# Optimization experiments

Measured on AMD Instinct MI355X. Metric: run time of the kernel, lower is better.

The kernel has to match this reference:

```python
import jax, jax.numpy as jnp
import numpy as np

N = 20000          # nodes (== virtual nodes, forced by scatter dim_size + residuals)
E = 240000         # edges
H = 256            # hidden_dim
SD = 128           # scalar_dim (mult of 0e in "128x0e+64x1o+32x2e")
FEAT = 128 + 64 * 3 + 32 * 5   # 480 = target_irreps dim
C = 4              # vn_channel


def _lin(key, din, dout):
    k1, k2 = jax.random.split(key)
    s = 1.0 / np.sqrt(din)
    w = jax.random.uniform(k1, (din, dout), jnp.float32, -s, s)
    b = jax.random.uniform(k2, (dout,), jnp.float32, -s, s)
    return w, b


def _mlp(x, w1, b1, w2, b2):
    # BaseMLP: Linear -> SiLU -> Linear (no norm, no residual, no last act)
    return jax.nn.silu(x @ w1 + b1) @ w2 + b2


def setup_inputs() -> dict:
    key = jax.random.key(0)
    ks = jax.random.split(key, 12)
    inp = {
        "node_feat": jax.random.normal(ks[0], (N, FEAT), jnp.float32),
        "node_pos": jax.random.normal(ks[1], (N, 3), jnp.float32),
        "vn_feat": jax.random.normal(ks[2], (N, H), jnp.float32),
        "vn_pos": jax.random.normal(ks[3], (N, 3 * C), jnp.float32),
        "edge_index": jax.random.randint(ks[4], (2, E), 0, N),
        "w_scalar": jax.random.normal(ks[5], (SD, SD), jnp.float32),  # e3nn o3.Linear 0e->0e path
    }
    mlps = {"cm": (SD + H + C * C, H), "vr": (H, C), "rv": (H, C * C),
            "ft": (H, H), "f2t": (H, SD), "vf": (H, H)}
    i = 6
    for name, (din, dout) in mlps.items():
        k1, k2 = jax.random.split(ks[i]); i += 1
        inp[name + "_w1"], inp[name + "_b1"] = _lin(k1, din, H)
        inp[name + "_w2"], inp[name + "_b2"] = _lin(k2, H, dout)
    return inp


def reference(node_feat, node_pos, vn_feat, vn_pos, edge_index, w_scalar,
              cm_w1, cm_b1, cm_w2, cm_b2, vr_w1, vr_b1, vr_w2, vr_b2,
              rv_w1, rv_b1, rv_w2, rv_b2, ft_w1, ft_b1, ft_w2, ft_b2,
              f2t_w1, f2t_b1, f2t_w2, f2t_b2, vf_w1, vf_b1, vf_w2, vf_b2):
    n = node_feat.shape[0]
    row, col = edge_index[0], edge_index[1]

    # e3nn o3.Linear(target_irreps -> SDx0e): single 0e->0e path, 1/sqrt(fan_in)
    nfs = (node_feat[:, :SD] @ w_scalar) * (1.0 / np.sqrt(SD))

    # per-edge relative positions between node pos (tiled to C channels) and vn pos
    d = (jnp.tile(node_pos[row], (1, C)) - vn_pos[col]).reshape(-1, C, 3)  # [E,C,3]

    # normalized gram matrix of the C difference vectors
    ip = jnp.einsum('ecj,ekj->eck', d, d).reshape(-1, C * C)
    ip = ip / jnp.maximum(jnp.linalg.norm(ip, axis=-1, keepdims=True), 1e-8)

    dn = d / jnp.maximum(jnp.linalg.norm(d, axis=-1, keepdims=True), 1e-8)  # [E,C,3]

    msg = _mlp(jnp.concatenate([nfs[row], vn_feat[col], ip], axis=1),
               cm_w1, cm_b1, cm_w2, cm_b2)                                   # [E,H]

    w_vr = _mlp(msg, vr_w1, vr_b1, vr_w2, vr_b2)                 # [E,C]
    w_rv = _mlp(msg, rv_w1, rv_b1, rv_w2, rv_b2).reshape(-1, C, C)

    inv = 1.0 / np.sqrt(C)
    # FCTP Cx1o (x) 1x0e -> 1x1o  (x2 == 1): weighted sum of the C vectors
    vr_upd = inv * jnp.einsum('ec,ecj->ej', w_vr, dn)            # [E,3]
    # FCTP Cx1o (x) 1x0e -> Cx1o on -dn
    rv_upd = inv * jnp.einsum('ecu,ecj->euj', w_rv, -dn).reshape(-1, 3 * C)  # [E,3C]

    cnt = jnp.maximum(jax.ops.segment_sum(jnp.ones((row.shape[0],), msg.dtype), row, n), 1.0)[:, None]
    agg_feat = jax.ops.segment_sum(msg, row, n) / cnt            # scatter_mean by row
    agg_vr = jax.ops.segment_sum(vr_upd, row, n) / cnt
    agg_rv = jax.ops.segment_sum(rv_upd, row, n) / cnt

    ds = _mlp(_mlp(agg_feat, ft_w1, ft_b1, ft_w2, ft_b2), f2t_w1, f2t_b1, f2t_w2, f2t_b2)
    node_feat_out = node_feat.at[:, :SD].add(ds)  # delta only hits the scalar (0e) block
    node_pos_out = node_pos + agg_vr
    vn_feat_out = vn_feat + _mlp(agg_feat, vf_w1, vf_b1, vf_w2, vf_b2)
    vn_pos_out = vn_pos + agg_rv
    return node_feat_out, node_pos_out, vn_feat_out, vn_pos_out
```

## Files before the change

kernel.cpp:

```cpp
#include <hip/hip_runtime.h>
#include <hip/hip_bf16.h>
#include <math.h>


#define FEAT 480
#define HDIM 256
#define SDIM 128
#define MSTR 264

#define OW1   0
#define OW2   106496
#define OVR1  172032
#define ORV1  237568
#define OVR2  303104
#define ORV2  307200
#define OFT1  311296
#define OFT2  376832
#define OF2T1 442368
#define OF2T2 507904
#define OVF1  540672
#define OVF2  606208
#define OWTOT 671744

#define NB_WPREP 2624
#define NB_VNB   5000
#define NB_NFS   625

typedef __attribute__((ext_vector_type(8))) short bf16x8;
typedef __attribute__((ext_vector_type(4))) float f32x4;

__device__ __forceinline__ float rcp_f(float x) {
    return __builtin_amdgcn_rcpf(x);
}
__device__ __forceinline__ float silu_f(float x) {
    return x * rcp_f(1.0f + __expf(-x));
}
__device__ __forceinline__ ushort f2b(float v) {
    __hip_bfloat16 h = __float2bfloat16(v);
    return *(ushort*)&h;
}
__device__ __forceinline__ float b2f(ushort u) {
    union { unsigned int i; float f; } c;
    c.i = ((unsigned int)u) << 16;
    return c.f;
}

#define KLOOP2(SRC, WP)                                                        \
    {                                                                          \
        _Pragma("unroll")                                                      \
        for (int mt = 0; mt < 4; ++mt)                                         \
            _Pragma("unroll")                                                  \
            for (int nt = 0; nt < 2; ++nt) acc[mt][nt] = (f32x4)0.f;           \
        __builtin_amdgcn_s_setprio(1);                                         \
        _Pragma("unroll")                                                      \
        for (int ks = 0; ks < 8; ++ks) {                                       \
            bf16x8 a_[4];                                                      \
            _Pragma("unroll")                                                  \
            for (int mt = 0; mt < 4; ++mt)                                     \
                a_[mt] = *(const bf16x8*)&(SRC)[(mt * 16 + lr) * MSTR + ks * 32 + lk * 8]; \
            _Pragma("unroll")                                                  \
            for (int nt = 0; nt < 2; ++nt) {                                   \
                const bf16x8 b = *(const bf16x8*)&(WP)[(size_t)(((wv * 2 + nt) * 8 + ks) * 512) + lane * 8]; \
                _Pragma("unroll")                                              \
                for (int mt = 0; mt < 4; ++mt)                                 \
                    acc[mt][nt] = __builtin_amdgcn_mfma_f32_16x16x32_bf16(a_[mt], b, acc[mt][nt], 0, 0, 0); \
            }                                                                  \
        }                                                                      \
        __builtin_amdgcn_s_setprio(0);                                         \
    }

#define EPI_SILU2(DST, BIAS)                                                   \
    _Pragma("unroll")                                                          \
    for (int nt = 0; nt < 2; ++nt) {                                           \
        const int col = colBase + nt * 16 + lr;                                \
        const float bb = (BIAS)[col];                                          \
        _Pragma("unroll")                                                      \
        for (int mt = 0; mt < 4; ++mt)                                         \
            _Pragma("unroll")                                                  \
            for (int r = 0; r < 4; ++r) {                                      \
                const int row = mt * 16 + lk * 4 + r;                          \
                (DST)[row * MSTR + col] = f2b(silu_f(acc[mt][nt][r] + bb));    \
            }                                                                  \
    }

#define KLOOP_FR(SRC, WP)                                                      \
    {                                                                          \
        _Pragma("unroll")                                                      \
        for (int mt = 0; mt < 2; ++mt)                                         \
            _Pragma("unroll")                                                  \
            for (int nt = 0; nt < 4; ++nt) accn[mt][nt] = (f32x4)0.f;          \
        _Pragma("unroll")                                                      \
        for (int ks = 0; ks < 8; ++ks) {                                       \
            const bf16x8 a0 = *(const bf16x8*)&(SRC)[lr * MSTR + ks * 32 + lk * 8];        \
            const bf16x8 a1 = *(const bf16x8*)&(SRC)[(lr + 16) * MSTR + ks * 32 + lk * 8]; \
            _Pragma("unroll")                                                  \
            for (int nt = 0; nt < 4; ++nt) {                                   \
                const bf16x8 b = *(const bf16x8*)&(WP)[(size_t)(((wv * 4 + nt) * 8 + ks) * 512) + lane * 8]; \
                accn[0][nt] = __builtin_amdgcn_mfma_f32_16x16x32_bf16(a0, b, accn[0][nt], 0, 0, 0); \
                accn[1][nt] = __builtin_amdgcn_mfma_f32_16x16x32_bf16(a1, b, accn[1][nt], 0, 0, 0); \
            }                                                                  \
        }                                                                      \
    }

#define EPI_SILUN(DST, BIAS)                                                   \
    _Pragma("unroll")                                                          \
    for (int nt = 0; nt < 4; ++nt) {                                           \
        const int col = colBase + nt * 16 + lr;                                \
        const float bb = (BIAS)[col];                                          \
        _Pragma("unroll")                                                      \
        for (int mt = 0; mt < 2; ++mt)                                         \
            _Pragma("unroll")                                                  \
            for (int r = 0; r < 4; ++r) {                                      \
                const int row = mt * 16 + lk * 4 + r;                          \
                (DST)[row * MSTR + col] = f2b(silu_f(accn[mt][nt][r] + bb));   \
            }                                                                  \
    }

__global__ __launch_bounds__(256) void k_prep(
    const float* __restrict__ w1, const float* __restrict__ w2,
    const float* __restrict__ vrw1, const float* __restrict__ rvw1,
    const float* __restrict__ vrw2, const float* __restrict__ rvw2,
    const float* __restrict__ ftw1, const float* __restrict__ ftw2,
    const float* __restrict__ f2tw1, const float* __restrict__ f2tw2,
    const float* __restrict__ vfw1, const float* __restrict__ vfw2,
    ushort* __restrict__ wb,
    const float* __restrict__ vn_feat, ushort* __restrict__ vnb,
    const float* __restrict__ node_feat, const float* __restrict__ w_scalar,
    ushort* __restrict__ nfsb,
    const int* __restrict__ eidx, int* __restrict__ cnt_i, int E)
{
    __shared__ float At[32][20];
    __shared__ float Wt[16][128];
    const int bid = blockIdx.x;
    const int t = threadIdx.x;

    if (bid < NB_WPREP) {
        const int idx = bid * 256 + t;
        ushort v;
        if (idx < OW2) {
            const int o = idx, f = o >> 9, l = (o >> 3) & 63, e = o & 7;
            const int nt = f / 13, ks = f % 13;
            const int col = nt * 16 + (l & 15);
            const int k = ks * 32 + ((l >> 4) << 3) + e;
            v = (k < 400) ? f2b(w1[(size_t)k * 256 + col]) : (ushort)0;
        } else if (idx < OVR1) {
            const int o = idx - OW2, f = o >> 9, l = (o >> 3) & 63, e = o & 7;
            const int col = (f >> 3) * 16 + (l & 15);
            const int k = (f & 7) * 32 + ((l >> 4) << 3) + e;
            v = f2b(w2[(size_t)k * 256 + col]);
        } else if (idx < ORV1) {
            const int o = idx - OVR1, f = o >> 9, l = (o >> 3) & 63, e = o & 7;
            const int col = (f >> 3) * 16 + (l & 15);
            const int k = (f & 7) * 32 + ((l >> 4) << 3) + e;
            v = f2b(vrw1[(size_t)k * 256 + col]);
        } else if (idx < OVR2) {
            const int o = idx - ORV1, f = o >> 9, l = (o >> 3) & 63, e = o & 7;
            const int col = (f >> 3) * 16 + (l & 15);
            const int k = (f & 7) * 32 + ((l >> 4) << 3) + e;
            v = f2b(rvw1[(size_t)k * 256 + col]);
        } else if (idx < ORV2) {
            const int o = idx - OVR2, f = o >> 9, l = (o >> 3) & 63, e = o & 7;
            const int col = l & 15;
            const int k = f * 32 + ((l >> 4) << 3) + e;
            v = (col < 4) ? f2b(vrw2[(size_t)k * 4 + col]) : (ushort)0;
        } else if (idx < OFT1) {
            const int o = idx - ORV2, f = o >> 9, l = (o >> 3) & 63, e = o & 7;
            const int col = l & 15;
            const int k = f * 32 + ((l >> 4) << 3) + e;
            v = f2b(rvw2[(size_t)k * 16 + col]);
        } else if (idx < OFT2) {
            const int o = idx - OFT1, f = o >> 9, l = (o >> 3) & 63, e = o & 7;
            const int col = (f >> 3) * 16 + (l & 15);
            const int k = (f & 7) * 32 + ((l >> 4) << 3) + e;
            v = f2b(ftw1[(size_t)k * 256 + col]);
        } else if (idx < OF2T1) {
            const int o = idx - OFT2, f = o >> 9, l = (o >> 3) & 63, e = o & 7;
            const int col = (f >> 3) * 16 + (l & 15);
            const int k = (f & 7) * 32 + ((l >> 4) << 3) + e;
            v = f2b(ftw2[(size_t)k * 256 + col]);
        } else if (idx < OF2T2) {
            const int o = idx - OF2T1, f = o >> 9, l = (o >> 3) & 63, e = o & 7;
            const int col = (f >> 3) * 16 + (l & 15);
            const int k = (f & 7) * 32 + ((l >> 4) << 3) + e;
            v = f2b(f2tw1[(size_t)k * 256 + col]);
        } else if (idx < OVF1) {
            const int o = idx - OF2T2, f = o >> 9, l = (o >> 3) & 63, e = o & 7;
            const int col = (f >> 3) * 16 + (l & 15);
            const int k = (f & 7) * 32 + ((l >> 4) << 3) + e;
            v = f2b(f2tw2[(size_t)k * 128 + col]);
        } else if (idx < OVF2) {
            const int o = idx - OVF1, f = o >> 9, l = (o >> 3) & 63, e = o & 7;
            const int col = (f >> 3) * 16 + (l & 15);
            const int k = (f & 7) * 32 + ((l >> 4) << 3) + e;
            v = f2b(vfw1[(size_t)k * 256 + col]);
        } else {
            const int o = idx - OVF2, f = o >> 9, l = (o >> 3) & 63, e = o & 7;
            const int col = (f >> 3) * 16 + (l & 15);
            const int k = (f & 7) * 32 + ((l >> 4) << 3) + e;
            v = f2b(vfw2[(size_t)k * 256 + col]);
        }
        wb[idx] = v;
    } else if (bid < NB_WPREP + NB_VNB) {
        const int i = (bid - NB_WPREP) * 256 + t;
        const float4 v = *(const float4*)&vn_feat[(size_t)i * 4];
        ushort4 o;
        o.x = f2b(v.x); o.y = f2b(v.y); o.z = f2b(v.z); o.w = f2b(v.w);
        *(ushort4*)&vnb[(size_t)i * 4] = o;
    } else if (bid < NB_WPREP + NB_VNB + NB_NFS) {
        const int m0 = (bid - NB_WPREP - NB_VNB) * 32;
        const int c4 = (t & 31) * 4;
        const int rg = t >> 5;
        float acc[4][4] = {};
        for (int k0 = 0; k0 < 128; k0 += 16) {
            if (t < 128) {
                const int r = t >> 2, kk = (t & 3) * 4;
                *(float4*)&At[r][kk] =
                    *(const float4*)&node_feat[(size_t)(m0 + r) * FEAT + k0 + kk];
            }
            #pragma unroll
            for (int i = 0; i < 2; ++i) {
                const int p  = t + i * 256;
                const int wr = p >> 5, wc = (p & 31) * 4;
                *(float4*)&Wt[wr][wc] =
                    *(const float4*)&w_scalar[(size_t)(k0 + wr) * SDIM + wc];
            }
            __syncthreads();
            #pragma unroll
            for (int kk = 0; kk < 16; ++kk) {
                const float4 w = *(const float4*)&Wt[kk][c4];
                #pragma unroll
                for (int j = 0; j < 4; ++j) {
                    const float a = At[rg * 4 + j][kk];
                    acc[j][0] = fmaf(a, w.x, acc[j][0]);
                    acc[j][1] = fmaf(a, w.y, acc[j][1]);
                    acc[j][2] = fmaf(a, w.z, acc[j][2]);
                    acc[j][3] = fmaf(a, w.w, acc[j][3]);
                }
            }
            __syncthreads();
        }
        const float s = 0.08838834764831845f;
        #pragma unroll
        for (int j = 0; j < 4; ++j) {
            ushort4 o;
            o.x = f2b(acc[j][0] * s); o.y = f2b(acc[j][1] * s);
            o.z = f2b(acc[j][2] * s); o.w = f2b(acc[j][3] * s);
            *(ushort4*)&nfsb[(size_t)(m0 + rg * 4 + j) * SDIM + c4] = o;
        }
    } else {
        const int e = (bid - NB_WPREP - NB_VNB - NB_NFS) * 256 + t;
        if (e < E) atomicAdd(&cnt_i[eidx[e]], 1);
    }
}

__global__ __launch_bounds__(1024) void k_scanA(
    const int* __restrict__ cnt_i, int* __restrict__ rowstart,
    float* __restrict__ cntf, int* __restrict__ bsum, int Nn)
{
    __shared__ int sh[1024];
    const int t = threadIdx.x;
    const int i = blockIdx.x * 1024 + t;
    const int v = (i < Nn) ? cnt_i[i] : 0;
    sh[t] = v;
    __syncthreads();
    for (int off = 1; off < 1024; off <<= 1) {
        const int add = (t >= off) ? sh[t - off] : 0;
        __syncthreads();
        sh[t] += add;
        __syncthreads();
    }
    if (i < Nn) {
        rowstart[i + 1] = sh[t];
        cntf[i] = fmaxf((float)v, 1.0f);
    }
    if (t == 1023) bsum[blockIdx.x] = sh[t];
}

__global__ __launch_bounds__(1024) void k_scanC(
    int* __restrict__ rowstart, const int* __restrict__ bsum, int Nn)
{
    __shared__ int carry_s;
    const int t = threadIdx.x;
    if (t == 0) {
        int s = 0;
        for (int b = 0; b < (int)blockIdx.x; ++b) s += bsum[b];
        carry_s = s;
    }
    __syncthreads();
    const int i = blockIdx.x * 1024 + t;
    if (i < Nn) rowstart[i + 1] += carry_s;
    if (i == 0) rowstart[0] = 0;
}

__global__ __launch_bounds__(256) void k_place(
    const int* __restrict__ eidx, const int* __restrict__ rowstart,
    int* __restrict__ cursor, int* __restrict__ elist, int E)
{
    const int e = blockIdx.x * 256 + threadIdx.x;
    if (e < E) {
        const int r = eidx[e];
        const int p = atomicAdd(&cursor[r], 1);
        elist[rowstart[r] + p] = e;
    }
}

__global__ __launch_bounds__(512, 4) void k_edge(
    const ushort* __restrict__ nfsb, const ushort* __restrict__ vnb,
    const float* __restrict__ node_pos, const float* __restrict__ vn_pos,
    const int* __restrict__ eidx, const int* __restrict__ elist,
    const ushort* __restrict__ wb,
    const float* __restrict__ b1, const float* __restrict__ b2,
    const float* __restrict__ vrb1, const float* __restrict__ vrb2,
    const float* __restrict__ rvb1, const float* __restrict__ rvb2,
    float* __restrict__ agg_feat, float* __restrict__ agg_vr,
    float* __restrict__ agg_rv, int E)
{
    __shared__ ushort Mg[64 * MSTR];
    __shared__ ushort Hd[64 * MSTR];
    __shared__ ushort ipB[64 * 16];
    __shared__ float dnS[64][12];
    __shared__ float wvrS[64][4];
    __shared__ float wrvS[64][16];
    __shared__ int rowi[64], coli[64];

    const int t  = threadIdx.x;
    const int nwg = E / 64;
    const int q = nwg >> 3, rr8 = nwg & 7;
    const int xcd = blockIdx.x & 7, pos = blockIdx.x >> 3;
    const int bswz = (xcd < rr8 ? xcd * (q + 1) : rr8 * (q + 1) + (xcd - rr8) * q) + pos;
    const int e0 = bswz * 64;
    const int wv = t >> 6;
    const int lane = t & 63;
    const int lr = lane & 15;
    const int lk = lane >> 4;
    const int colBase = wv * 32;

    if (t < 64) {
        const int e = elist[e0 + t];
        const int r = eidx[e];
        const int c = eidx[E + e];
        rowi[t] = r; coli[t] = c;
        const float px = node_pos[r * 3 + 0];
        const float py = node_pos[r * 3 + 1];
        const float pz = node_pos[r * 3 + 2];
        float d[4][3];
        #pragma unroll
        for (int ch = 0; ch < 4; ++ch) {
            d[ch][0] = px - vn_pos[(size_t)c * 12 + ch * 3 + 0];
            d[ch][1] = py - vn_pos[(size_t)c * 12 + ch * 3 + 1];
            d[ch][2] = pz - vn_pos[(size_t)c * 12 + ch * 3 + 2];
        }
        float ss = 0.f, ipv[16];
        #pragma unroll
        for (int ci = 0; ci < 4; ++ci)
            #pragma unroll
            for (int ck = 0; ck < 4; ++ck) {
                const float v = d[ci][0]*d[ck][0] + d[ci][1]*d[ck][1] + d[ci][2]*d[ck][2];
                ipv[ci * 4 + ck] = v; ss += v * v;
            }
        const float inrm = rcp_f(fmaxf(sqrtf(ss), 1e-8f));
        #pragma unroll
        for (int i = 0; i < 16; ++i) ipB[t * 16 + i] = f2b(ipv[i] * inrm);
        #pragma unroll
        for (int ch = 0; ch < 4; ++ch) {
            const float nn = sqrtf(d[ch][0]*d[ch][0] + d[ch][1]*d[ch][1] + d[ch][2]*d[ch][2]);
            const float s = rcp_f(fmaxf(nn, 1e-8f));
            dnS[t][ch * 3 + 0] = d[ch][0] * s;
            dnS[t][ch * 3 + 1] = d[ch][1] * s;
            dnS[t][ch * 3 + 2] = d[ch][2] * s;
        }
    }
    __syncthreads();

    const ushort* nA[4]; const ushort* vA[4];
    #pragma unroll
    for (int mt = 0; mt < 4; ++mt) {
        nA[mt] = nfsb + (size_t)rowi[mt * 16 + lr] * SDIM + lk * 8;
        vA[mt] = vnb  + (size_t)coli[mt * 16 + lr] * HDIM + lk * 8;
    }
    const ushort* w1t = wb + OW1;

    f32x4 acc[4][2];

    #pragma unroll
    for (int mt = 0; mt < 4; ++mt)
        #pragma unroll
        for (int nt = 0; nt < 2; ++nt) acc[mt][nt] = (f32x4)0.f;
    __builtin_amdgcn_s_setprio(1);
    #pragma unroll
    for (int ks = 0; ks < 13; ++ks) {
        bf16x8 a_[4];
        #pragma unroll
        for (int mt = 0; mt < 4; ++mt) {
            if (ks < 4)       a_[mt] = *(const bf16x8*)(nA[mt] + ks * 32);
            else if (ks < 12) a_[mt] = *(const bf16x8*)(vA[mt] + ks * 32 - 128);
            else if (lk < 2)  a_[mt] = *(const bf16x8*)&ipB[(mt * 16 + lr) * 16 + lk * 8];
            else              a_[mt] = (bf16x8)(short)0;
        }
        #pragma unroll
        for (int nt = 0; nt < 2; ++nt) {
            const bf16x8 b = *(const bf16x8*)&w1t[(size_t)(((wv * 2 + nt) * 13 + ks) * 512) + lane * 8];
            #pragma unroll
            for (int mt = 0; mt < 4; ++mt)
                acc[mt][nt] = __builtin_amdgcn_mfma_f32_16x16x32_bf16(a_[mt], b, acc[mt][nt], 0, 0, 0);
        }
    }
    __builtin_amdgcn_s_setprio(0);
    EPI_SILU2(Hd, b1);
    __syncthreads();

    KLOOP2(Hd, wb + OW2);
    #pragma unroll
    for (int nt = 0; nt < 2; ++nt) {
        const int col = colBase + nt * 16 + lr;
        const float bb = b2[col];
        #pragma unroll
        for (int mt = 0; mt < 4; ++mt)
            #pragma unroll
            for (int r = 0; r < 4; ++r) {
                const int row = mt * 16 + lk * 4 + r;
                Mg[row * MSTR + col] = f2b(acc[mt][nt][r] + bb);
            }
    }
    __syncthreads();

    {
        const int col = t & 255;
        const int r0 = (t >> 8) * 32;
        float s = 0.f;
        int prev = rowi[r0];
        for (int r = r0; r < r0 + 32; ++r) {
            const int rr = rowi[r];
            if (rr != prev) {
                atomicAdd(&agg_feat[(size_t)prev * HDIM + col], s);
                s = 0.f; prev = rr;
            }
            s += b2f(Mg[r * MSTR + col]);
        }
        atomicAdd(&agg_feat[(size_t)prev * HDIM + col], s);
    }

    KLOOP2(Mg, wb + OVR1);
    EPI_SILU2(Hd, vrb1);

    KLOOP2(Mg, wb + ORV1);
    __syncthreads();
    #pragma unroll
    for (int nt = 0; nt < 2; ++nt) {
        const int col = colBase + nt * 16 + lr;
        const float br = rvb1[col];
        #pragma unroll
        for (int mt = 0; mt < 4; ++mt)
            #pragma unroll
            for (int r = 0; r < 4; ++r) {
                const int row = mt * 16 + lk * 4 + r;
                Mg[row * MSTR + col] = f2b(silu_f(acc[mt][nt][r] + br));
            }
    }
    __syncthreads();

    if ((wv & 3) == 0) {
        const int rb = (wv >> 2) * 32;
        const ushort* vrw2t = wb + OVR2;
        f32x4 a2[2]; a2[0] = (f32x4)0.f; a2[1] = (f32x4)0.f;
        #pragma unroll
        for (int ks = 0; ks < 8; ++ks) {
            const bf16x8 a0 = *(const bf16x8*)&Hd[(rb + lr) * MSTR + ks * 32 + lk * 8];
            const bf16x8 a1 = *(const bf16x8*)&Hd[(rb + 16 + lr) * MSTR + ks * 32 + lk * 8];
            const bf16x8 b  = *(const bf16x8*)&vrw2t[(size_t)(ks * 512) + lane * 8];
            a2[0] = __builtin_amdgcn_mfma_f32_16x16x32_bf16(a0, b, a2[0], 0, 0, 0);
            a2[1] = __builtin_amdgcn_mfma_f32_16x16x32_bf16(a1, b, a2[1], 0, 0, 0);
        }
        if (lr < 4) {
            const float bb = vrb2[lr];
            #pragma unroll
            for (int mt = 0; mt < 2; ++mt)
                #pragma unroll
                for (int r = 0; r < 4; ++r)
                    wvrS[rb + mt * 16 + lk * 4 + r][lr] = a2[mt][r] + bb;
        }
    } else if ((wv & 3) == 1) {
        const int rb = (wv >> 2) * 32;
        const ushort* rvw2t = wb + ORV2;
        f32x4 a2[2]; a2[0] = (f32x4)0.f; a2[1] = (f32x4)0.f;
        #pragma unroll
        for (int ks = 0; ks < 8; ++ks) {
            const bf16x8 a0 = *(const bf16x8*)&Mg[(rb + lr) * MSTR + ks * 32 + lk * 8];
            const bf16x8 a1 = *(const bf16x8*)&Mg[(rb + 16 + lr) * MSTR + ks * 32 + lk * 8];
            const bf16x8 b  = *(const bf16x8*)&rvw2t[(size_t)(ks * 512) + lane * 8];
            a2[0] = __builtin_amdgcn_mfma_f32_16x16x32_bf16(a0, b, a2[0], 0, 0, 0);
            a2[1] = __builtin_amdgcn_mfma_f32_16x16x32_bf16(a1, b, a2[1], 0, 0, 0);
        }
        const float bb = rvb2[lr];
        #pragma unroll
        for (int mt = 0; mt < 2; ++mt)
            #pragma unroll
            for (int r = 0; r < 4; ++r)
                wrvS[rb + mt * 16 + lk * 4 + r][lr] = a2[mt][r] + bb;
    }
    __syncthreads();

    if (t < 64) {
        float wvv[4], wrr[16], dn[12], ev[15];
        #pragma unroll
        for (int c = 0; c < 4; ++c)  wvv[c] = wvrS[t][c];
        #pragma unroll
        for (int i = 0; i < 16; ++i) wrr[i] = wrvS[t][i];
        #pragma unroll
        for (int i = 0; i < 12; ++i) dn[i]  = dnS[t][i];
        #pragma unroll
        for (int j = 0; j < 3; ++j) {
            float v = 0.f;
            #pragma unroll
            for (int c = 0; c < 4; ++c) v = fmaf(wvv[c], dn[c * 3 + j], v);
            ev[j] = 0.5f * v;
        }
        #pragma unroll
        for (int u = 0; u < 4; ++u)
            #pragma unroll
            for (int j = 0; j < 3; ++j) {
                float v = 0.f;
                #pragma unroll
                for (int c = 0; c < 4; ++c) v = fmaf(wrr[c * 4 + u], dn[c * 3 + j], v);
                ev[3 + u * 3 + j] = -0.5f * v;
            }
        #pragma unroll
        for (int i = 0; i < 15; ++i) wrvS[t][i] = ev[i];
    }
    __syncthreads();

    if ((t & 255) < 15) {
        const int comp = t & 255;
        const int r0 = (t >> 8) * 32;
        float s = 0.f;
        int prev = rowi[r0];
        for (int r = r0; r < r0 + 32; ++r) {
            const int rr = rowi[r];
            if (rr != prev) {
                if (comp < 3) atomicAdd(&agg_vr[(size_t)prev * 3 + comp], s);
                else          atomicAdd(&agg_rv[(size_t)prev * 12 + (comp - 3)], s);
                s = 0.f; prev = rr;
            }
            s += wrvS[r][comp];
        }
        if (comp < 3) atomicAdd(&agg_vr[(size_t)prev * 3 + comp], s);
        else          atomicAdd(&agg_rv[(size_t)prev * 12 + (comp - 3)], s);
    }
}

__global__ __launch_bounds__(256, 4) void k_node(
    const float* __restrict__ node_feat, const float* __restrict__ node_pos,
    const float* __restrict__ vn_feat, const float* __restrict__ vn_pos,
    const float* __restrict__ agg_feat, const float* __restrict__ agg_vr,
    const float* __restrict__ agg_rv, const float* __restrict__ cntf,
    const ushort* __restrict__ wb,
    const float* __restrict__ ftb1, const float* __restrict__ ftb2,
    const float* __restrict__ f2tb1, const float* __restrict__ f2tb2,
    const float* __restrict__ vfb1, const float* __restrict__ vfb2,
    float* __restrict__ out, int Nn)
{
    __shared__ ushort Ab[32 * MSTR];
    __shared__ ushort Hd[32 * MSTR];
    __shared__ float rc[32];
    const int t  = threadIdx.x;
    const int n0 = blockIdx.x * 32;
    const int wv = t >> 6;
    const int lane = t & 63;
    const int lr = lane & 15;
    const int lk = lane >> 4;
    const int colBase = wv * 64;

    float* nf_out = out;
    float* np_out = out + (size_t)Nn * FEAT;
    float* vf_out = np_out + (size_t)Nn * 3;
    float* vp_out = vf_out + (size_t)Nn * HDIM;

    if (t < 32) rc[t] = rcp_f(fmaxf(cntf[n0 + t], 1.0f));
    __syncthreads();
    #pragma unroll
    for (int i = 0; i < 8; ++i) {
        const int p = t + i * 256;
        const int r = p >> 6, cc = (p & 63) * 4;
        float4 v = *(const float4*)&agg_feat[(size_t)(n0 + r) * HDIM + cc];
        const float s = rc[r];
        ushort4 o;
        o.x = f2b(v.x * s); o.y = f2b(v.y * s);
        o.z = f2b(v.z * s); o.w = f2b(v.w * s);
        *(ushort4*)&Ab[r * MSTR + cc] = o;
    }
    __syncthreads();

    f32x4 accn[2][4];

    KLOOP_FR(Ab, wb + OVF1);
    EPI_SILUN(Hd, vfb1);
    __syncthreads();
    KLOOP_FR(Hd, wb + OVF2);
    #pragma unroll
    for (int nt = 0; nt < 4; ++nt) {
        const int col = colBase + nt * 16 + lr;
        const float bb = vfb2[col];
        #pragma unroll
        for (int mt = 0; mt < 2; ++mt)
            #pragma unroll
            for (int r = 0; r < 4; ++r) {
                const int row = mt * 16 + lk * 4 + r;
                const size_t o = (size_t)(n0 + row) * HDIM + col;
                vf_out[o] = vn_feat[o] + accn[mt][nt][r] + bb;
            }
    }
    __syncthreads();

    KLOOP_FR(Ab, wb + OFT1);
    EPI_SILUN(Hd, ftb1);
    __syncthreads();
    KLOOP_FR(Hd, wb + OFT2);
    #pragma unroll
    for (int nt = 0; nt < 4; ++nt) {
        const int col = colBase + nt * 16 + lr;
        const float bb = ftb2[col];
        #pragma unroll
        for (int mt = 0; mt < 2; ++mt)
            #pragma unroll
            for (int r = 0; r < 4; ++r) {
                const int row = mt * 16 + lk * 4 + r;
                Ab[row * MSTR + col] = f2b(accn[mt][nt][r] + bb);
            }
    }
    __syncthreads();

    KLOOP_FR(Ab, wb + OF2T1);
    EPI_SILUN(Hd, f2tb1);
    __syncthreads();
    {
        const ushort* w2p = wb + OF2T2;
        f32x4 a2[2][2];
        #pragma unroll
        for (int mt = 0; mt < 2; ++mt)
            #pragma unroll
            for (int nt = 0; nt < 2; ++nt) a2[mt][nt] = (f32x4)0.f;
        #pragma unroll
        for (int ks = 0; ks < 8; ++ks) {
            const int k0 = ks * 32 + lk * 8;
            const bf16x8 a0 = *(const bf16x8*)&Hd[lr * MSTR + k0];
            const bf16x8 a1 = *(const bf16x8*)&Hd[(lr + 16) * MSTR + k0];
            const bf16x8 w0 = *(const bf16x8*)&w2p[(size_t)(((wv * 2 + 0) * 8 + ks) * 512) + lane * 8];
            const bf16x8 w1v = *(const bf16x8*)&w2p[(size_t)(((wv * 2 + 1) * 8 + ks) * 512) + lane * 8];
            a2[0][0] = __builtin_amdgcn_mfma_f32_16x16x32_bf16(a0, w0, a2[0][0], 0, 0, 0);
            a2[1][0] = __builtin_amdgcn_mfma_f32_16x16x32_bf16(a1, w0, a2[1][0], 0, 0, 0);
            a2[0][1] = __builtin_amdgcn_mfma_f32_16x16x32_bf16(a0, w1v, a2[0][1], 0, 0, 0);
            a2[1][1] = __builtin_amdgcn_mfma_f32_16x16x32_bf16(a1, w1v, a2[1][1], 0, 0, 0);
        }
        #pragma unroll
        for (int nt = 0; nt < 2; ++nt) {
            const int col = wv * 32 + nt * 16 + lr;
            const float bb = f2tb2[col];
            #pragma unroll
            for (int mt = 0; mt < 2; ++mt)
                #pragma unroll
                for (int r = 0; r < 4; ++r) {
                    const int row = mt * 16 + lk * 4 + r;
                    const size_t o = (size_t)(n0 + row) * FEAT + col;
                    nf_out[o] = node_feat[o] + a2[mt][nt][r] + bb;
                }
        }
    }

    for (int p = t; p < 32 * 88; p += 256) {
        const int r = p / 88;
        const int cc = 128 + (p % 88) * 4;
        const size_t o = (size_t)(n0 + r) * FEAT + cc;
        *(float4*)&nf_out[o] = *(const float4*)&node_feat[o];
    }
    if (t < 32) {
        const int n = n0 + t;
        const float s = rc[t];
        #pragma unroll
        for (int j = 0; j < 3; ++j)
            np_out[(size_t)n * 3 + j] = node_pos[(size_t)n * 3 + j] + agg_vr[(size_t)n * 3 + j] * s;
        #pragma unroll
        for (int j = 0; j < 12; ++j)
            vp_out[(size_t)n * 12 + j] = vn_pos[(size_t)n * 12 + j] + agg_rv[(size_t)n * 12 + j] * s;
    }
}

extern "C" void kernel_launch(void* const* d_in, const int* in_sizes, int n_in,
                              void* d_out, int out_size, void* d_ws, size_t ws_size,
                              hipStream_t stream)
{
    (void)n_in; (void)out_size; (void)ws_size;
    const float* node_feat = (const float*)d_in[0];
    const float* node_pos  = (const float*)d_in[1];
    const float* vn_feat   = (const float*)d_in[2];
    const float* vn_pos    = (const float*)d_in[3];
    const int*   eidx      = (const int*)d_in[4];
    const float* w_scalar  = (const float*)d_in[5];
    const float* cm_w1  = (const float*)d_in[6];
    const float* cm_b1  = (const float*)d_in[7];
    const float* cm_w2  = (const float*)d_in[8];
    const float* cm_b2  = (const float*)d_in[9];
    const float* vr_w1  = (const float*)d_in[10];
    const float* vr_b1  = (const float*)d_in[11];
    const float* vr_w2  = (const float*)d_in[12];
    const float* vr_b2  = (const float*)d_in[13];
    const float* rv_w1  = (const float*)d_in[14];
    const float* rv_b1  = (const float*)d_in[15];
    const float* rv_w2  = (const float*)d_in[16];
    const float* rv_b2  = (const float*)d_in[17];
    const float* ft_w1  = (const float*)d_in[18];
    const float* ft_b1  = (const float*)d_in[19];
    const float* ft_w2  = (const float*)d_in[20];
    const float* ft_b2  = (const float*)d_in[21];
    const float* f2t_w1 = (const float*)d_in[22];
    const float* f2t_b1 = (const float*)d_in[23];
    const float* f2t_w2 = (const float*)d_in[24];
    const float* f2t_b2 = (const float*)d_in[25];
    const float* vf_w1  = (const float*)d_in[26];
    const float* vf_b1  = (const float*)d_in[27];
    const float* vf_w2  = (const float*)d_in[28];
    const float* vf_b2  = (const float*)d_in[29];

    const int Nn = in_sizes[0] / FEAT;
    const int E  = in_sizes[4] / 2;

    float* ws       = (float*)d_ws;
    float* agg_feat = ws;
    float* agg_vr   = agg_feat + (size_t)Nn * HDIM;
    float* agg_rv   = agg_vr   + (size_t)Nn * 3;
    float* cntf     = agg_rv   + (size_t)Nn * 12;
    int*   cnt_i    = (int*)(cntf + Nn);
    int*   cursor   = cnt_i + Nn;
    int*   rowstart = cursor + Nn;
    int*   bsum     = rowstart + Nn + 8;
    int*   elist    = bsum + 64;
    ushort* nfsb = (ushort*)(elist + E);
    ushort* vnb  = nfsb + (size_t)Nn * SDIM;
    ushort* wb   = vnb  + (size_t)Nn * HDIM;

    const size_t zero_bytes = (size_t)Nn * (HDIM + 3 + 12 + 1 + 2) * sizeof(float);
    hipMemsetAsync(agg_feat, 0, zero_bytes, stream);

    const int eg = (E + 255) / 256;
    const int sb = (Nn + 1023) / 1024;
    k_prep<<<NB_WPREP + NB_VNB + NB_NFS + eg, 256, 0, stream>>>(
        cm_w1, cm_w2, vr_w1, rv_w1, vr_w2, rv_w2,
        ft_w1, ft_w2, f2t_w1, f2t_w2, vf_w1, vf_w2, wb,
        vn_feat, vnb, node_feat, w_scalar, nfsb,
        eidx, cnt_i, E);
    k_scanA<<<sb, 1024, 0, stream>>>(cnt_i, rowstart, cntf, bsum, Nn);
    k_scanC<<<sb, 1024, 0, stream>>>(rowstart, bsum, Nn);
    k_place<<<eg, 256, 0, stream>>>(eidx, rowstart, cursor, elist, E);
    k_edge<<<E / 64, 512, 0, stream>>>(nfsb, vnb, node_pos, vn_pos, eidx, elist,
                                       wb, cm_b1, cm_b2, vr_b1, vr_b2, rv_b1, rv_b2,
                                       agg_feat, agg_vr, agg_rv, E);
    k_node<<<Nn / 32, 256, 0, stream>>>(node_feat, node_pos, vn_feat, vn_pos,
                                        agg_feat, agg_vr, agg_rv, cntf, wb,
                                        ft_b1, ft_b2, f2t_b1, f2t_b2, vf_b1, vf_b2,
                                        (float*)d_out, Nn);
}
```

Before: 410.9 us.

## Shrink edge tile to 48 rows and trim LDS to raise edge-kernel occupancy

Changes the edge kernel's per-block edge tile from 64 to 48 so its LDS footprint shrinks: dn vectors stay in registers, ipB aliases the message buffer, and the small head outputs are stored as bf16. Launch bounds go from 4 to 6 blocks per SM to allow more concurrent blocks. The vr and rv second-layer MFMA work now runs on a single wave each instead of two. The smaller tile means fewer MFMA rows per weight-fragment load and more blocks in total, and the extra bf16 rounding of intermediate weights slightly lowers precision.

```diff
diff --git a/kernel.cpp b/kernel.cpp
--- a/kernel.cpp
+++ b/kernel.cpp
@@ -7,6 +7,7 @@
 #define HDIM 256
 #define SDIM 128
 #define MSTR 264
+#define EB   48
 
 #define OW1   0
 #define OW2   106496
@@ -48,21 +49,21 @@
 #define KLOOP2(SRC, WP)                                                        \
     {                                                                          \
         _Pragma("unroll")                                                      \
-        for (int mt = 0; mt < 4; ++mt)                                         \
+        for (int mt = 0; mt < 3; ++mt)                                         \
             _Pragma("unroll")                                                  \
             for (int nt = 0; nt < 2; ++nt) acc[mt][nt] = (f32x4)0.f;           \
         __builtin_amdgcn_s_setprio(1);                                         \
         _Pragma("unroll")                                                      \
         for (int ks = 0; ks < 8; ++ks) {                                       \
-            bf16x8 a_[4];                                                      \
+            bf16x8 a_[3];                                                      \
             _Pragma("unroll")                                                  \
-            for (int mt = 0; mt < 4; ++mt)                                     \
+            for (int mt = 0; mt < 3; ++mt)                                     \
                 a_[mt] = *(const bf16x8*)&(SRC)[(mt * 16 + lr) * MSTR + ks * 32 + lk * 8]; \
             _Pragma("unroll")                                                  \
             for (int nt = 0; nt < 2; ++nt) {                                   \
                 const bf16x8 b = *(const bf16x8*)&(WP)[(size_t)(((wv * 2 + nt) * 8 + ks) * 512) + lane * 8]; \
                 _Pragma("unroll")                                              \
-                for (int mt = 0; mt < 4; ++mt)                                 \
+                for (int mt = 0; mt < 3; ++mt)                                 \
                     acc[mt][nt] = __builtin_amdgcn_mfma_f32_16x16x32_bf16(a_[mt], b, acc[mt][nt], 0, 0, 0); \
             }                                                                  \
         }                                                                      \
@@ -75,7 +76,7 @@
         const int col = colBase + nt * 16 + lr;                                \
         const float bb = (BIAS)[col];                                          \
         _Pragma("unroll")                                                      \
-        for (int mt = 0; mt < 4; ++mt)                                         \
+        for (int mt = 0; mt < 3; ++mt)                                         \
             _Pragma("unroll")                                                  \
             for (int r = 0; r < 4; ++r) {                                      \
                 const int row = mt * 16 + lk * 4 + r;                          \
@@ -304,7 +305,7 @@
     }
 }
 
-__global__ __launch_bounds__(512, 4) void k_edge(
+__global__ __launch_bounds__(512, 6) void k_edge(
     const ushort* __restrict__ nfsb, const ushort* __restrict__ vnb,
     const float* __restrict__ node_pos, const float* __restrict__ vn_pos,
     const int* __restrict__ eidx, const int* __restrict__ elist,
@@ -315,27 +316,28 @@
     float* __restrict__ agg_feat, float* __restrict__ agg_vr,
     float* __restrict__ agg_rv, int E)
 {
-    __shared__ ushort Mg[64 * MSTR];
-    __shared__ ushort Hd[64 * MSTR];
-    __shared__ ushort ipB[64 * 16];
-    __shared__ float dnS[64][12];
-    __shared__ float wvrS[64][4];
-    __shared__ float wrvS[64][16];
-    __shared__ int rowi[64], coli[64];
+    __shared__ ushort Mg[EB * MSTR];
+    __shared__ ushort Hd[EB * MSTR];
+    __shared__ ushort wvrS[EB * 4];
+    __shared__ ushort wrvS[EB * 16];
+    __shared__ int rowi[EB], coli[EB];
 
     const int t  = threadIdx.x;
-    const int nwg = E / 64;
+    const int nwg = E / EB;
     const int q = nwg >> 3, rr8 = nwg & 7;
     const int xcd = blockIdx.x & 7, pos = blockIdx.x >> 3;
     const int bswz = (xcd < rr8 ? xcd * (q + 1) : rr8 * (q + 1) + (xcd - rr8) * q) + pos;
-    const int e0 = bswz * 64;
+    const int e0 = bswz * EB;
     const int wv = t >> 6;
     const int lane = t & 63;
     const int lr = lane & 15;
     const int lk = lane >> 4;
     const int colBase = wv * 32;
-
-    if (t < 64) {
+    ushort* ipB = Mg;
+
+    float dnr[12];
+
+    if (t < EB) {
         const int e = elist[e0 + t];
         const int r = eidx[e];
         const int c = eidx[E + e];
@@ -365,33 +367,33 @@
         for (int ch = 0; ch < 4; ++ch) {
             const float nn = sqrtf(d[ch][0]*d[ch][0] + d[ch][1]*d[ch][1] + d[ch][2]*d[ch][2]);
             const float s = rcp_f(fmaxf(nn, 1e-8f));
-            dnS[t][ch * 3 + 0] = d[ch][0] * s;
-            dnS[t][ch * 3 + 1] = d[ch][1] * s;
-            dnS[t][ch * 3 + 2] = d[ch][2] * s;
-        }
-    }
-    __syncthreads();
-
-    const ushort* nA[4]; const ushort* vA[4];
+            dnr[ch * 3 + 0] = d[ch][0] * s;
+            dnr[ch * 3 + 1] = d[ch][1] * s;
+            dnr[ch * 3 + 2] = d[ch][2] * s;
+        }
+    }
+    __syncthreads();
+
+    const ushort* nA[3]; const ushort* vA[3];
     #pragma unroll
-    for (int mt = 0; mt < 4; ++mt) {
+    for (int mt = 0; mt < 3; ++mt) {
         nA[mt] = nfsb + (size_t)rowi[mt * 16 + lr] * SDIM + lk * 8;
         vA[mt] = vnb  + (size_t)coli[mt * 16 + lr] * HDIM + lk * 8;
     }
     const ushort* w1t = wb + OW1;
 
-    f32x4 acc[4][2];
+    f32x4 acc[3][2];
 
     #pragma unroll
-    for (int mt = 0; mt < 4; ++mt)
+    for (int mt = 0; mt < 3; ++mt)
         #pragma unroll
         for (int nt = 0; nt < 2; ++nt) acc[mt][nt] = (f32x4)0.f;
     __builtin_amdgcn_s_setprio(1);
     #pragma unroll
     for (int ks = 0; ks < 13; ++ks) {
-        bf16x8 a_[4];
-        #pragma unroll
-        for (int mt = 0; mt < 4; ++mt) {
+        bf16x8 a_[3];
+        #pragma unroll
+        for (int mt = 0; mt < 3; ++mt) {
             if (ks < 4)       a_[mt] = *(const bf16x8*)(nA[mt] + ks * 32);
             else if (ks < 12) a_[mt] = *(const bf16x8*)(vA[mt] + ks * 32 - 128);
             else if (lk < 2)  a_[mt] = *(const bf16x8*)&ipB[(mt * 16 + lr) * 16 + lk * 8];
@@ -401,7 +403,7 @@
         for (int nt = 0; nt < 2; ++nt) {
             const bf16x8 b = *(const bf16x8*)&w1t[(size_t)(((wv * 2 + nt) * 13 + ks) * 512) + lane * 8];
             #pragma unroll
-            for (int mt = 0; mt < 4; ++mt)
+            for (int mt = 0; mt < 3; ++mt)
                 acc[mt][nt] = __builtin_amdgcn_mfma_f32_16x16x32_bf16(a_[mt], b, acc[mt][nt], 0, 0, 0);
         }
     }
@@ -415,7 +417,7 @@
         const int col = colBase + nt * 16 + lr;
         const float bb = b2[col];
         #pragma unroll
-        for (int mt = 0; mt < 4; ++mt)
+        for (int mt = 0; mt < 3; ++mt)
             #pragma unroll
             for (int r = 0; r < 4; ++r) {
                 const int row = mt * 16 + lk * 4 + r;
@@ -426,10 +428,10 @@
 
     {
         const int col = t & 255;
-        const int r0 = (t >> 8) * 32;
+        const int r0 = (t >> 8) * 24;
         float s = 0.f;
         int prev = rowi[r0];
-        for (int r = r0; r < r0 + 32; ++r) {
+        for (int r = r0; r < r0 + 24; ++r) {
             const int rr = rowi[r];
             if (rr != prev) {
                 atomicAdd(&agg_feat[(size_t)prev * HDIM + col], s);
@@ -450,7 +452,7 @@
         const int col = colBase + nt * 16 + lr;
         const float br = rvb1[col];
         #pragma unroll
-        for (int mt = 0; mt < 4; ++mt)
+        for (int mt = 0; mt < 3; ++mt)
             #pragma unroll
             for (int r = 0; r < 4; ++r) {
                 const int row = mt * 16 + lk * 4 + r;
@@ -459,60 +461,62 @@
     }
     __syncthreads();
 
-    if ((wv & 3) == 0) {
-        const int rb = (wv >> 2) * 32;
+    if (wv == 0) {
         const ushort* vrw2t = wb + OVR2;
-        f32x4 a2[2]; a2[0] = (f32x4)0.f; a2[1] = (f32x4)0.f;
+        f32x4 a2[3];
+        #pragma unroll
+        for (int mt = 0; mt < 3; ++mt) a2[mt] = (f32x4)0.f;
         #pragma unroll
         for (int ks = 0; ks < 8; ++ks) {
-            const bf16x8 a0 = *(const bf16x8*)&Hd[(rb + lr) * MSTR + ks * 32 + lk * 8];
-            const bf16x8 a1 = *(const bf16x8*)&Hd[(rb + 16 + lr) * MSTR + ks * 32 + lk * 8];
-            const bf16x8 b  = *(const bf16x8*)&vrw2t[(size_t)(ks * 512) + lane * 8];
-            a2[0] = __builtin_amdgcn_mfma_f32_16x16x32_bf16(a0, b, a2[0], 0, 0, 0);
-            a2[1] = __builtin_amdgcn_mfma_f32_16x16x32_bf16(a1, b, a2[1], 0, 0, 0);
+            const bf16x8 b = *(const bf16x8*)&vrw2t[(size_t)(ks * 512) + lane * 8];
+            #pragma unroll
+            for (int mt = 0; mt < 3; ++mt) {
+                const bf16x8 a = *(const bf16x8*)&Hd[(mt * 16 + lr) * MSTR + ks * 32 + lk * 8];
+                a2[mt] = __builtin_amdgcn_mfma_f32_16x16x32_bf16(a, b, a2[mt], 0, 0, 0);
+            }
         }
         if (lr < 4) {
             const float bb = vrb2[lr];
             #pragma unroll
-            for (int mt = 0; mt < 2; ++mt)
+            for (int mt = 0; mt < 3; ++mt)
                 #pragma unroll
                 for (int r = 0; r < 4; ++r)
-                    wvrS[rb + mt * 16 + lk * 4 + r][lr] = a2[mt][r] + bb;
-        }
-    } else if ((wv & 3) == 1) {
-        const int rb = (wv >> 2) * 32;
+                    wvrS[(mt * 16 + lk * 4 + r) * 4 + lr] = f2b(a2[mt][r] + bb);
+        }
+    } else if (wv == 1) {
         const ushort* rvw2t = wb + ORV2;
-        f32x4 a2[2]; a2[0] = (f32x4)0.f; a2[1] = (f32x4)0.f;
+        f32x4 a2[3];
+        #pragma unroll
+        for (int mt = 0; mt < 3; ++mt) a2[mt] = (f32x4)0.f;
         #pragma unroll
         for (int ks = 0; ks < 8; ++ks) {
-            const bf16x8 a0 = *(const bf16x8*)&Mg[(rb + lr) * MSTR + ks * 32 + lk * 8];
-            const bf16x8 a1 = *(const bf16x8*)&Mg[(rb + 16 + lr) * MSTR + ks * 32 + lk * 8];
-            const bf16x8 b  = *(const bf16x8*)&rvw2t[(size_t)(ks * 512) + lane * 8];
-            a2[0] = __builtin_amdgcn_mfma_f32_16x16x32_bf16(a0, b, a2[0], 0, 0, 0);
-            a2[1] = __builtin_amdgcn_mfma_f32_16x16x32_bf16(a1, b, a2[1], 0, 0, 0);
+            const bf16x8 b = *(const bf16x8*)&rvw2t[(size_t)(ks * 512) + lane * 8];
+            #pragma unroll
+            for (int mt = 0; mt < 3; ++mt) {
+                const bf16x8 a = *(const bf16x8*)&Mg[(mt * 16 + lr) * MSTR + ks * 32 + lk * 8];
+                a2[mt] = __builtin_amdgcn_mfma_f32_16x16x32_bf16(a, b, a2[mt], 0, 0, 0);
+            }
         }
         const float bb = rvb2[lr];
         #pragma unroll
-        for (int mt = 0; mt < 2; ++mt)
+        for (int mt = 0; mt < 3; ++mt)
             #pragma unroll
             for (int r = 0; r < 4; ++r)
-                wrvS[rb + mt * 16 + lk * 4 + r][lr] = a2[mt][r] + bb;
-    }
-    __syncthreads();
-
-    if (t < 64) {
-        float wvv[4], wrr[16], dn[12], ev[15];
-        #pragma unroll
-        for (int c = 0; c < 4; ++c)  wvv[c] = wvrS[t][c];
-        #pragma unroll
-        for (int i = 0; i < 16; ++i) wrr[i] = wrvS[t][i];
-        #pragma unroll
-        for (int i = 0; i < 12; ++i) dn[i]  = dnS[t][i];
+                wrvS[(mt * 16 + lk * 4 + r) * 16 + lr] = f2b(a2[mt][r] + bb);
+    }
+    __syncthreads();
+
+    if (t < EB) {
+        float wvv[4], wrr[16], ev[15];
+        #pragma unroll
+        for (int c = 0; c < 4; ++c)  wvv[c] = b2f(wvrS[t * 4 + c]);
+        #pragma unroll
+        for (int i = 0; i < 16; ++i) wrr[i] = b2f(wrvS[t * 16 + i]);
         #pragma unroll
         for (int j = 0; j < 3; ++j) {
             float v = 0.f;
             #pragma unroll
-            for (int c = 0; c < 4; ++c) v = fmaf(wvv[c], dn[c * 3 + j], v);
+            for (int c = 0; c < 4; ++c) v = fmaf(wvv[c], dnr[c * 3 + j], v);
             ev[j] = 0.5f * v;
         }
         #pragma unroll
@@ -521,27 +525,27 @@
             for (int j = 0; j < 3; ++j) {
                 float v = 0.f;
                 #pragma unroll
-                for (int c = 0; c < 4; ++c) v = fmaf(wrr[c * 4 + u], dn[c * 3 + j], v);
+                for (int c = 0; c < 4; ++c) v = fmaf(wrr[c * 4 + u], dnr[c * 3 + j], v);
                 ev[3 + u * 3 + j] = -0.5f * v;
             }
         #pragma unroll
-        for (int i = 0; i < 15; ++i) wrvS[t][i] = ev[i];
+        for (int i = 0; i < 15; ++i) wrvS[t * 16 + i] = f2b(ev[i]);
     }
     __syncthreads();
 
     if ((t & 255) < 15) {
         const int comp = t & 255;
-        const int r0 = (t >> 8) * 32;
+        const int r0 = (t >> 8) * 24;
         float s = 0.f;
         int prev = rowi[r0];
-        for (int r = r0; r < r0 + 32; ++r) {
+        for (int r = r0; r < r0 + 24; ++r) {
             const int rr = rowi[r];
             if (rr != prev) {
                 if (comp < 3) atomicAdd(&agg_vr[(size_t)prev * 3 + comp], s);
                 else          atomicAdd(&agg_rv[(size_t)prev * 12 + (comp - 3)], s);
                 s = 0.f; prev = rr;
             }
-            s += wrvS[r][comp];
+            s += b2f(wrvS[r * 16 + comp]);
         }
         if (comp < 3) atomicAdd(&agg_vr[(size_t)prev * 3 + comp], s);
         else          atomicAdd(&agg_rv[(size_t)prev * 12 + (comp - 3)], s);
@@ -750,7 +754,7 @@
     k_scanA<<<sb, 1024, 0, stream>>>(cnt_i, rowstart, cntf, bsum, Nn);
     k_scanC<<<sb, 1024, 0, stream>>>(rowstart, bsum, Nn);
     k_place<<<eg, 256, 0, stream>>>(eidx, rowstart, cursor, elist, E);
-    k_edge<<<E / 64, 512, 0, stream>>>(nfsb, vnb, node_pos, vn_pos, eidx, elist,
+    k_edge<<<E / EB, 512, 0, stream>>>(nfsb, vnb, node_pos, vn_pos, eidx, elist,
                                        wb, cm_b1, cm_b2, vr_b1, vr_b2, rv_b1, rv_b2,
                                        agg_feat, agg_vr, agg_rv, E);
     k_node<<<Nn / 32, 256, 0, stream>>>(node_feat, node_pos, vn_feat, vn_pos,
```

New measurement: 434.9 us. 1.06x slower.
